# Performance work log

Hardware: AMD Instinct MI355X
Metric: run time of the kernel (lower is better)

The kernel has to match this reference:

```python
import jax, jax.numpy as jnp
import numpy as np

B, S, D, H, L = 32, 1024, 512, 8, 4
DH = D // H
FF = D            # dim_feedforward == hidden_dim in the original ctor call
LOC_D, TD_D = 16, 8
TD_EMB = 3        # time_dist_embed_dim
POI = 21          # poi vocab
POI_EMB = 3
ADDR_IN = 1 + POI_EMB
FC = 32           # fc_hidden_dim
NEG = -1e9


def setup_inputs() -> dict:
    key = jax.random.key(0)
    ks = jax.random.split(key, 20)
    g = lambda i, shape, s=0.02: jax.random.normal(ks[i], shape, jnp.float32) * s
    return {
        "addr": jax.random.normal(ks[0], (B, 1), jnp.float32),
        "loc_dense_seq": jax.random.normal(ks[1], (B, S, LOC_D), jnp.float32),
        "time_dist_seq": jax.random.normal(ks[2], (B, S, TD_D), jnp.float32),
        "Wtd": g(3, (TD_D, TD_EMB)), "btd": jnp.zeros((TD_EMB,), jnp.float32),
        "Wemb": g(4, (LOC_D + TD_EMB, D)), "bemb": jnp.zeros((D,), jnp.float32),
        "Wqkv": g(5, (L, D, 3 * D)), "bqkv": jnp.zeros((L, 3 * D), jnp.float32),
        "Wo": g(6, (L, D, D)), "bo": jnp.zeros((L, D), jnp.float32),
        "ln1_g": jnp.ones((L, D), jnp.float32), "ln1_b": jnp.zeros((L, D), jnp.float32),
        "W1": g(7, (L, D, FF)), "b1": jnp.zeros((L, FF), jnp.float32),
        "W2": g(8, (L, FF, D)), "b2": jnp.zeros((L, D), jnp.float32),
        "ln2_g": jnp.ones((L, D), jnp.float32), "ln2_b": jnp.zeros((L, D), jnp.float32),
        "poi_emb": g(9, (POI, POI_EMB), 1.0),
        "Wa": g(10, (ADDR_IN, FC)), "ba": jnp.zeros((FC,), jnp.float32),
        "Wout": g(11, (D, FC)),
        "Wcomb": g(12, (FC, 1)),
        "addr_type": jax.random.randint(ks[13], (B, 1), 0, POI),
        "data_length": jax.random.randint(ks[14], (B,), 1, S + 1),
    }


def _ln(x, g, b, eps=1e-5):
    m = x.mean(-1, keepdims=True)
    v = ((x - m) ** 2).mean(-1, keepdims=True)
    return (x - m) / jnp.sqrt(v + eps) * g + b


def reference(addr, loc_dense_seq, time_dist_seq, Wtd, btd, Wemb, bemb, Wqkv,
              bqkv, Wo, bo, ln1_g, ln1_b, W1, b1, W2, b2, ln2_g, ln2_b,
              poi_emb, Wa, ba, Wout, Wcomb, addr_type, data_length):
    valid = jnp.arange(S)[None, :] < data_length[:, None]            # [B,S]
    td = time_dist_seq @ Wtd + btd                                   # [B,S,3]
    x = jnp.concatenate([loc_dense_seq, td], axis=-1) @ Wemb + bemb  # [B,S,D]
    scale = 1.0 / jnp.sqrt(jnp.float32(DH))
    for l in range(L):  # post-norm TransformerEncoderLayer (relu, eval/no-dropout)
        qkv = x @ Wqkv[l] + bqkv[l]
        q, k, v = jnp.split(qkv, 3, axis=-1)
        q = q.reshape(B, S, H, DH)
        k = k.reshape(B, S, H, DH)
        v = v.reshape(B, S, H, DH)
        scores = jnp.einsum('bqhd,bkhd->bhqk', q, k) * scale
        scores = jnp.where(valid[:, None, None, :], scores, NEG)     # mask padded keys
        attn = jax.nn.softmax(scores, axis=-1)
        ctx = jnp.einsum('bhqk,bkhd->bqhd', attn, v).reshape(B, S, D)
        x = _ln(x + ctx @ Wo[l] + bo[l], ln1_g[l], ln1_b[l])
        ff = jax.nn.relu(x @ W1[l] + b1[l]) @ W2[l] + b2[l]
        x = _ln(x + ff, ln2_g[l], ln2_b[l])
    # per-sample addr branch (vectorized over the original python loop)
    addr_inp = jnp.concatenate([addr, poi_emb[addr_type[:, 0]]], axis=-1)  # [B,4]
    a = addr_inp @ Wa + ba                                                 # [B,FC]
    o = (jnp.tanh(x @ Wout + a[:, None, :]) @ Wcomb)[..., 0]              # [B,S]
    logits = jnp.where(valid, o, NEG)
    logp = jax.nn.log_softmax(logits, axis=1)  # log_softmax over valid positions only
    return jnp.where(valid, logp, 0.0)
```

## Files before the change

### kernel.cpp

```cpp
#include <hip/hip_runtime.h>
#include <stdint.h>


typedef unsigned short u16;
typedef __attribute__((ext_vector_type(8))) short short8;
typedef __attribute__((ext_vector_type(4))) float f32x4;

constexpr int Bn = 32, Sn = 1024, Dn = 512, Ln = 4;
constexpr int BS = Bn * Sn;

__device__ __forceinline__ float b2f(u16 u) {
    union { uint32_t i; float f; } v; v.i = ((uint32_t)u) << 16; return v.f;
}
__device__ __forceinline__ u16 f2b(float f) {
    union { float f; uint32_t i; } v; v.f = f;
    uint32_t r = v.i + 0x7fffu + ((v.i >> 16) & 1u);
    return (u16)(r >> 16);
}
__device__ __forceinline__ float getf(const void* p, size_t i, int F) {
    return F ? ((const float*)p)[i] : b2f(((const u16*)p)[i]);
}
__device__ __forceinline__ void cp16(void* lds, const void* g) {
    __builtin_amdgcn_global_load_lds(
        (__attribute__((address_space(1))) void*)(uintptr_t)g,
        (__attribute__((address_space(3))) void*)(uint32_t)(uintptr_t)lds,
        16, 0, 0);
}
__device__ __forceinline__ float asf(uint32_t u) {
    union { uint32_t i; float f; } v; v.i = u; return v.f;
}

__global__ __launch_bounds__(256)
void detect_kernel(const void* loc, int* flag)
{
    __shared__ int cnt;
    if (threadIdx.x == 0) cnt = 0;
    __syncthreads();
    const u16* p = (const u16*)loc;
    int c = 0;
    for (int i = threadIdx.x; i < 2048; i += 256) {
        const float v = b2f(p[i]);
        if (!(fabsf(v) <= 100.0f)) c++;
    }
    atomicAdd(&cnt, c);
    __syncthreads();
    if (threadIdx.x == 0) *flag = (cnt >= 64) ? 1 : 0;
}

__global__ __launch_bounds__(256)
void gemm_bt(const u16* __restrict__ A, const u16* __restrict__ Bt,
             const void* __restrict__ bias, int boff, u16* __restrict__ C,
             int N, int K, int relu, const int* __restrict__ flagp,
             const int* __restrict__ dlen)
{
    __shared__ __align__(16) u16 As[128 * 32];
    __shared__ __align__(16) u16 Bs[128 * 32];
    const int bn0 = blockIdx.x * 128, bm0 = blockIdx.y * 128;
    if ((bm0 & 1023) >= dlen[bm0 >> 10]) return;
    const int F = *flagp;
    const int tid = threadIdx.x;
    const int lane = tid & 63, w = tid >> 6;
    const int wm = w >> 1, wn = w & 1;
    const int quad = lane >> 4, l16 = lane & 15;

    const f32x4 vzero = {0.f, 0.f, 0.f, 0.f};
    f32x4 acc[4][4];
#pragma unroll
    for (int i = 0; i < 4; i++)
#pragma unroll
        for (int j = 0; j < 4; j++) acc[i][j] = vzero;

    const int i0 = tid, i1 = tid + 256;
    const u16* a0 = A + (size_t)(bm0 + (i0 >> 2)) * K + (i0 & 3) * 8;
    const u16* a1 = A + (size_t)(bm0 + (i1 >> 2)) * K + (i1 & 3) * 8;
    const u16* b0 = Bt + (size_t)(bn0 + (i0 >> 2)) * K + (i0 & 3) * 8;
    const u16* b1 = Bt + (size_t)(bn0 + (i1 >> 2)) * K + (i1 & 3) * 8;

    for (int k0 = 0; k0 < K; k0 += 32) {
        cp16(As + i0 * 8, a0 + k0);
        cp16(As + i1 * 8, a1 + k0);
        cp16(Bs + i0 * 8, b0 + k0);
        cp16(Bs + i1 * 8, b1 + k0);
        __syncthreads();
        short8 af[4], bfr[4];
#pragma unroll
        for (int t = 0; t < 4; t++)
            af[t] = *(const short8*)&As[(wm * 64 + t * 16 + l16) * 32 + quad * 8];
#pragma unroll
        for (int t = 0; t < 4; t++)
            bfr[t] = *(const short8*)&Bs[(wn * 64 + t * 16 + l16) * 32 + quad * 8];
#pragma unroll
        for (int tm = 0; tm < 4; tm++)
#pragma unroll
            for (int tn = 0; tn < 4; tn++)
                acc[tm][tn] = __builtin_amdgcn_mfma_f32_16x16x32_bf16(
                    af[tm], bfr[tn], acc[tm][tn], 0, 0, 0);
        __syncthreads();
    }
#pragma unroll
    for (int tm = 0; tm < 4; tm++)
#pragma unroll
        for (int tn = 0; tn < 4; tn++) {
            const int col = bn0 + wn * 64 + tn * 16 + l16;
            const float bv = getf(bias, (size_t)boff + col, F);
#pragma unroll
            for (int r = 0; r < 4; r++) {
                const int row = bm0 + wm * 64 + tm * 16 + quad * 4 + r;
                float v = acc[tm][tn][r] + bv;
                if (relu) v = fmaxf(v, 0.0f);
                C[(size_t)row * N + col] = f2b(v);
            }
        }
}

__global__ __launch_bounds__(256)
void attn_kernel(const u16* __restrict__ qkv, const int* __restrict__ dlen,
                 u16* __restrict__ ctx)
{
    const int id = blockIdx.x;
    const int qt = id >> 8, bh = id & 255;
    const int h = bh & 7, b = bh >> 3;
    const int len = dlen[b];
    if (qt * 128 >= len) return;
    const int tid = threadIdx.x, lane = tid & 63, w = tid >> 6;
    const int quad = lane >> 4, l16 = lane & 15;
    __shared__ __align__(16) u16 Vt[2][64 * 72];
    __shared__ __align__(16) u16 Pl[4][32 * 72];
    u16* Plw = Pl[w];
    const int sw = l16 & 3;
    const size_t rs = 3 * Dn;
    const u16* base = qkv + (size_t)b * Sn * rs;
    const int q0 = qt * 128 + w * 32;
    constexpr float SC = 0.18033688011112043f;

    short8 qf[2][2];
#pragma unroll
    for (int sub = 0; sub < 2; sub++)
#pragma unroll
        for (int s = 0; s < 2; s++)
            qf[sub][s] = *(const short8*)(base + (size_t)(q0 + sub * 16 + l16) * rs
                                          + h * 64 + quad * 8 + 32 * s);

    const int key2 = (tid & 31) * 2, f0 = (tid >> 5) * 8;
    const u16* vsrc = base + 2 * Dn + h * 64 + f0;
    short8 v0 = *(const short8*)(vsrc + (size_t)key2 * rs);
    short8 v1 = *(const short8*)(vsrc + (size_t)(key2 + 1) * rs);

    short8 ones;
#pragma unroll
    for (int j = 0; j < 8; j++) ones[j] = (short)0x3F80;

    const f32x4 vzero = {0.f, 0.f, 0.f, 0.f};
    f32x4 O[2][4], lacc[2];
#pragma unroll
    for (int sub = 0; sub < 2; sub++) {
        lacc[sub] = vzero;
#pragma unroll
        for (int t = 0; t < 4; t++) O[sub][t] = vzero;
    }

    const int nkt = (len + 63) >> 6;
    int buf = 0;
    for (int kt = 0; kt < nkt; kt++) {
        const int k0 = kt * 64;
        u16* Vb = Vt[buf];
#pragma unroll
        for (int j = 0; j < 8; j++)
            *(uint32_t*)&Vb[(f0 + j) * 72 + key2] =
                (uint32_t)(u16)v0[j] | ((uint32_t)(u16)v1[j] << 16);
        __syncthreads();
        if (kt + 1 < nkt) {
            const u16* nv = vsrc + (size_t)(k0 + 64 + key2) * rs;
            v0 = *(const short8*)nv;
            v1 = *(const short8*)(nv + rs);
        }
        short8 kf[4][2];
#pragma unroll
        for (int tn = 0; tn < 4; tn++) {
            const u16* kp = base + (size_t)(k0 + tn * 16 + l16) * rs + Dn
                            + h * 64 + quad * 8;
            kf[tn][0] = *(const short8*)kp;
            kf[tn][1] = *(const short8*)(kp + 32);
        }
        const bool full = (k0 + 64 <= len);
#pragma unroll
        for (int sub = 0; sub < 2; sub++) {
            f32x4 sacc[4];
#pragma unroll
            for (int tn = 0; tn < 4; tn++) {
                f32x4 z = vzero;
                z = __builtin_amdgcn_mfma_f32_16x16x32_bf16(kf[tn][0], qf[sub][0], z, 0, 0, 0);
                sacc[tn] = __builtin_amdgcn_mfma_f32_16x16x32_bf16(kf[tn][1], qf[sub][1], z, 0, 0, 0);
            }
            const int prow = (sub * 16 + l16) * 72;
#pragma unroll
            for (int tn = 0; tn < 4; tn++) {
                float p[4];
                if (full) {
#pragma unroll
                    for (int r = 0; r < 4; r++) p[r] = exp2f(sacc[tn][r] * SC);
                } else {
                    const int kb = k0 + tn * 16 + quad * 4;
#pragma unroll
                    for (int r = 0; r < 4; r++)
                        p[r] = (kb + r < len) ? exp2f(sacc[tn][r] * SC) : 0.0f;
                }
                uint2 pk;
                pk.x = (__float_as_uint(p[0]) >> 16) | (__float_as_uint(p[1]) & 0xFFFF0000u);
                pk.y = (__float_as_uint(p[2]) >> 16) | (__float_as_uint(p[3]) & 0xFFFF0000u);
                *(uint2*)&Plw[prow + (((tn ^ sw) << 4) + quad * 4)] = pk;
            }
        }
        __builtin_amdgcn_wave_barrier();
#pragma unroll
        for (int s = 0; s < 2; s++) {
            const int tnr = ((quad >> 1) + 2 * s) ^ sw;
            short8 pf0 = *(const short8*)&Plw[(l16) * 72 + (tnr << 4) + (quad & 1) * 8];
            short8 pf1 = *(const short8*)&Plw[(16 + l16) * 72 + (tnr << 4) + (quad & 1) * 8];
            lacc[0] = __builtin_amdgcn_mfma_f32_16x16x32_bf16(pf0, ones, lacc[0], 0, 0, 0);
            lacc[1] = __builtin_amdgcn_mfma_f32_16x16x32_bf16(pf1, ones, lacc[1], 0, 0, 0);
#pragma unroll
            for (int t = 0; t < 4; t++) {
                short8 vf = *(const short8*)&Vb[(t * 16 + l16) * 72 + quad * 8 + 32 * s];
                O[0][t] = __builtin_amdgcn_mfma_f32_16x16x32_bf16(pf0, vf, O[0][t], 0, 0, 0);
                O[1][t] = __builtin_amdgcn_mfma_f32_16x16x32_bf16(pf1, vf, O[1][t], 0, 0, 0);
            }
        }
        __builtin_amdgcn_wave_barrier();
        buf ^= 1;
    }
#pragma unroll
    for (int sub = 0; sub < 2; sub++)
#pragma unroll
        for (int r = 0; r < 4; r++) {
            const float inv = 1.0f / lacc[sub][r];
            const int q = q0 + sub * 16 + quad * 4 + r;
#pragma unroll
            for (int t = 0; t < 4; t++)
                ctx[(size_t)(b * Sn + q) * Dn + h * 64 + t * 16 + l16] =
                    f2b(O[sub][t][r] * inv);
        }
}

__global__ __launch_bounds__(256)
void ln_res(u16* __restrict__ x, const u16* __restrict__ t,
            const void* __restrict__ g, const void* __restrict__ bta, int off,
            const int* __restrict__ flagp, const int* __restrict__ dlen)
{
    const int w = threadIdx.x >> 6, lane = threadIdx.x & 63;
    const size_t row = (size_t)blockIdx.x * 4 + w;
    if ((int)(row & 1023) >= dlen[row >> 10]) return;
    const int F = *flagp;
    u16* xp = x + row * Dn;
    const u16* tp = t + row * Dn;
    const int c0 = lane * 8;
    short8 xv = *(const short8*)(xp + c0);
    short8 tv = *(const short8*)(tp + c0);
    float v[8]; float s = 0.f;
#pragma unroll
    for (int i = 0; i < 8; i++) {
        v[i] = b2f((u16)xv[i]) + b2f((u16)tv[i]);
        s += v[i];
    }
#pragma unroll
    for (int o = 1; o < 64; o <<= 1) s += __shfl_xor(s, o, 64);
    const float mean = s * (1.0f / 512.0f);
    float q = 0.f;
#pragma unroll
    for (int i = 0; i < 8; i++) { const float d = v[i] - mean; q += d * d; }
#pragma unroll
    for (int o = 1; o < 64; o <<= 1) q += __shfl_xor(q, o, 64);
    const float inv = rsqrtf(q * (1.0f / 512.0f) + 1e-5f);
    short8 ov;
#pragma unroll
    for (int i = 0; i < 8; i++)
        ov[i] = (short)f2b((v[i] - mean) * inv * getf(g, off + c0 + i, F)
                           + getf(bta, off + c0 + i, F));
    *(short8*)(xp + c0) = ov;
}

__global__ __launch_bounds__(256)
void embed_kernel(const void* __restrict__ loc, const void* __restrict__ tds,
                  const void* __restrict__ Wtd, const void* __restrict__ btd,
                  const void* __restrict__ Wemb, const void* __restrict__ bemb,
                  u16* __restrict__ x, const int* __restrict__ flagp,
                  const int* __restrict__ dlen)
{
    const int token = blockIdx.x;
    if ((token & 1023) >= dlen[token >> 10]) return;
    const int F = *flagp;
    const int tid = threadIdx.x;
    __shared__ float inv[19];
    if (tid < 16) {
        inv[tid] = getf(loc, (size_t)token * 16 + tid, F);
    } else if (tid < 19) {
        const int e = tid - 16;
        float a = getf(btd, e, F);
        for (int j = 0; j < 8; j++)
            a += getf(tds, (size_t)token * 8 + j, F) * getf(Wtd, j * 3 + e, F);
        inv[tid] = a;
    }
    __syncthreads();
    for (int d = tid; d < Dn; d += 256) {
        float a = getf(bemb, d, F);
#pragma unroll
        for (int i = 0; i < 19; i++) a += inv[i] * getf(Wemb, (size_t)i * Dn + d, F);
        x[(size_t)token * Dn + d] = f2b(a);
    }
}

__global__ __launch_bounds__(256)
void transpose_w(const void* __restrict__ src, u16* __restrict__ dst,
                 int K, int N, const int* __restrict__ flagp)
{
    const int F = *flagp;
    __shared__ u16 tile[32][33];
    const size_t ls = (size_t)K * N;
    const size_t sb = (size_t)blockIdx.z * ls;
    u16* d = dst + blockIdx.z * ls;
    const int tx = threadIdx.x & 31, ty = threadIdx.x >> 5;
    const int n0 = blockIdx.x * 32, k0 = blockIdx.y * 32;
#pragma unroll
    for (int i = 0; i < 32; i += 8)
        tile[ty + i][tx] = f2b(getf(src, sb + (size_t)(k0 + ty + i) * N + n0 + tx, F));
    __syncthreads();
#pragma unroll
    for (int i = 0; i < 32; i += 8)
        d[(size_t)(n0 + ty + i) * K + k0 + tx] = tile[tx][ty + i];
}

__global__ __launch_bounds__(256)
void final_proj(const u16* __restrict__ x, const void* __restrict__ Wout,
                const void* __restrict__ Wcomb, const void* __restrict__ addr,
                const void* __restrict__ poi, const int* __restrict__ atype,
                const void* __restrict__ Wa, const void* __restrict__ ba,
                float* __restrict__ logits, const int* __restrict__ flagp,
                const int* __restrict__ dlen)
{
    const int F = *flagp;
    __shared__ float xs[8][512];
    __shared__ __align__(8) u16 wlds[32 * 516];
    const int tid = threadIdx.x;
    const int t0 = blockIdx.x * 8;
    for (int i = tid; i < 8 * 512; i += 256) {
        const int tk = i >> 9, d = i & 511;
        xs[tk][d] = b2f(x[(size_t)(t0 + tk) * Dn + d]);
    }
    for (int i = tid; i < 16384; i += 256) {
        const int k = i >> 5, j = i & 31;
        wlds[j * 516 + k] = F ? f2b(((const float*)Wout)[(size_t)k * 32 + j])
                              : ((const u16*)Wout)[(size_t)k * 32 + j];
    }
    __syncthreads();
    const int half = tid >> 5, j = tid & 31;
    const int token = t0 + half;
    const int b = token >> 10;
    if ((token & 1023) >= dlen[b]) return;
    const int ty = atype[b];
    float a = getf(ba, j, F) + getf(addr, b, F) * getf(Wa, j, F);
#pragma unroll
    for (int e = 0; e < 3; e++)
        a += getf(poi, ty * 3 + e, F) * getf(Wa, (1 + e) * 32 + j, F);
    float s = a;
    const u16* wj = wlds + j * 516;
    const float* xr = xs[half];
#pragma unroll 4
    for (int k = 0; k < 512; k += 4) {
        const uint2 wv = *(const uint2*)&wj[k];
        s += xr[k]     * asf(wv.x << 16);
        s += xr[k + 1] * asf(wv.x & 0xFFFF0000u);
        s += xr[k + 2] * asf(wv.y << 16);
        s += xr[k + 3] * asf(wv.y & 0xFFFF0000u);
    }
    float o = tanhf(s) * getf(Wcomb, j, F);
#pragma unroll
    for (int off = 1; off < 32; off <<= 1) o += __shfl_xor(o, off, 64);
    if (j == 0) logits[token] = o;
}

__global__ __launch_bounds__(256)
void lsm_kernel(const float* __restrict__ logits, const int* __restrict__ dlen,
                float* __restrict__ out)
{
    const int b = blockIdx.x, tid = threadIdx.x;
    const int len = dlen[b];
    const float* lp = logits + (size_t)b * Sn;
    __shared__ float wA[4], wB[4];
    float mx = -3e38f;
    for (int s = tid; s < Sn; s += 256) if (s < len) mx = fmaxf(mx, lp[s]);
#pragma unroll
    for (int o = 1; o < 64; o <<= 1) mx = fmaxf(mx, __shfl_xor(mx, o, 64));
    if ((tid & 63) == 0) wA[tid >> 6] = mx;
    __syncthreads();
    mx = fmaxf(fmaxf(wA[0], wA[1]), fmaxf(wA[2], wA[3]));
    float sm = 0.f;
    for (int s = tid; s < Sn; s += 256) if (s < len) sm += __expf(lp[s] - mx);
#pragma unroll
    for (int o = 1; o < 64; o <<= 1) sm += __shfl_xor(sm, o, 64);
    if ((tid & 63) == 0) wB[tid >> 6] = sm;
    __syncthreads();
    const float lse = mx + __logf(wB[0] + wB[1] + wB[2] + wB[3]);
    for (int s = tid; s < Sn; s += 256)
        out[(size_t)b * Sn + s] = (s < len) ? (lp[s] - lse) : 0.0f;
}

extern "C" void kernel_launch(void* const* d_in, const int* in_sizes, int n_in,
                              void* d_out, int out_size, void* d_ws, size_t ws_size,
                              hipStream_t stream) {
    const void* addr  = d_in[0];
    const void* loc   = d_in[1];
    const void* tds   = d_in[2];
    const void* Wtd   = d_in[3];
    const void* btd   = d_in[4];
    const void* Wemb  = d_in[5];
    const void* bemb  = d_in[6];
    const void* Wqkv  = d_in[7];
    const void* bqkv  = d_in[8];
    const void* Wo    = d_in[9];
    const void* bo    = d_in[10];
    const void* ln1g  = d_in[11];
    const void* ln1b  = d_in[12];
    const void* W1    = d_in[13];
    const void* b1    = d_in[14];
    const void* W2    = d_in[15];
    const void* b2    = d_in[16];
    const void* ln2g  = d_in[17];
    const void* ln2b  = d_in[18];
    const void* poi   = d_in[19];
    const void* Wa    = d_in[20];
    const void* ba    = d_in[21];
    const void* Wout  = d_in[22];
    const void* Wcomb = d_in[23];
    const int* atype  = (const int*)d_in[24];
    const int* dlen   = (const int*)d_in[25];

    char* base = (char*)d_ws;
    u16*   xb    = (u16*)(base);
    u16*   qkvb  = (u16*)(base + 33554432ull);
    u16*   ctxb  = (u16*)(base + 134217728ull);
    u16*   tb    = (u16*)(base + 167772160ull);
    u16*   wqkvT = (u16*)(base + 201326592ull);
    u16*   woT   = (u16*)(base + 207618048ull);
    u16*   w1T   = (u16*)(base + 209715200ull);
    u16*   w2T   = (u16*)(base + 211812352ull);
    float* logit = (float*)(base + 213909504ull);
    int*   flag  = (int*)  (base + 214040576ull);
    if (ws_size < 214040592ull) return;

    detect_kernel<<<1, 256, 0, stream>>>(loc, flag);

    transpose_w<<<dim3(48, 16, 4), 256, 0, stream>>>(Wqkv, wqkvT, 512, 1536, flag);
    transpose_w<<<dim3(16, 16, 4), 256, 0, stream>>>(Wo,   woT,   512, 512, flag);
    transpose_w<<<dim3(16, 16, 4), 256, 0, stream>>>(W1,   w1T,   512, 512, flag);
    transpose_w<<<dim3(16, 16, 4), 256, 0, stream>>>(W2,   w2T,   512, 512, flag);

    embed_kernel<<<BS, 256, 0, stream>>>(loc, tds, Wtd, btd, Wemb, bemb, xb, flag, dlen);

    for (int l = 0; l < Ln; l++) {
        gemm_bt<<<dim3(12, 256), 256, 0, stream>>>(
            xb, wqkvT + (size_t)l * 1536 * 512, bqkv, l * 1536, qkvb, 1536, 512, 0, flag, dlen);
        attn_kernel<<<2048, 256, 0, stream>>>(qkvb, dlen, ctxb);
        gemm_bt<<<dim3(4, 256), 256, 0, stream>>>(
            ctxb, woT + (size_t)l * 512 * 512, bo, l * 512, tb, 512, 512, 0, flag, dlen);
        ln_res<<<BS / 4, 256, 0, stream>>>(xb, tb, ln1g, ln1b, l * 512, flag, dlen);
        gemm_bt<<<dim3(4, 256), 256, 0, stream>>>(
            xb, w1T + (size_t)l * 512 * 512, b1, l * 512, ctxb, 512, 512, 1, flag, dlen);
        gemm_bt<<<dim3(4, 256), 256, 0, stream>>>(
            ctxb, w2T + (size_t)l * 512 * 512, b2, l * 512, tb, 512, 512, 0, flag, dlen);
        ln_res<<<BS / 4, 256, 0, stream>>>(xb, tb, ln2g, ln2b, l * 512, flag, dlen);
    }

    final_proj<<<BS / 8, 256, 0, stream>>>(xb, Wout, Wcomb, addr, poi, atype,
                                           Wa, ba, logit, flag, dlen);
    lsm_kernel<<<Bn, 256, 0, stream>>>(logit, dlen, (float*)d_out);
}
```

Before: 1.747 ms.

## Prefetch K fragments one tile ahead, reverse query-tile order, skip padded final blocks

The attention kernel now double-buffers K fragments in registers, loading the next key tile's K alongside the V prefetch so global-load latency overlaps the current tile's MFMA work. Query tiles are dispatched in reverse order so the longest-running tiles start first, which improves load balance across the variable sequence lengths. The final projection kernel returns early for blocks whose first token lies past the valid length, so no shared-memory staging is done for them. The K double buffer raises register pressure and may reduce occupancy.

```diff
diff --git a/kernel.cpp b/kernel.cpp
--- a/kernel.cpp
+++ b/kernel.cpp
@@ -118,7 +118,8 @@
                  u16* __restrict__ ctx)
 {
     const int id = blockIdx.x;
-    const int qt = id >> 8, bh = id & 255;
+    const int qt = 7 - (id >> 8);
+    const int bh = id & 255;
     const int h = bh & 7, b = bh >> 3;
     const int len = dlen[b];
     if (qt * 128 >= len) return;
@@ -146,6 +147,15 @@
     short8 v0 = *(const short8*)(vsrc + (size_t)key2 * rs);
     short8 v1 = *(const short8*)(vsrc + (size_t)(key2 + 1) * rs);
 
+    const u16* kbase = base + Dn + h * 64 + quad * 8;
+    short8 kfb[2][4][2];
+#pragma unroll
+    for (int tn = 0; tn < 4; tn++) {
+        const u16* kp = kbase + (size_t)(tn * 16 + l16) * rs;
+        kfb[0][tn][0] = *(const short8*)kp;
+        kfb[0][tn][1] = *(const short8*)(kp + 32);
+    }
+
     short8 ones;
 #pragma unroll
     for (int j = 0; j < 8; j++) ones[j] = (short)0x3F80;
@@ -160,7 +170,7 @@
     }
 
     const int nkt = (len + 63) >> 6;
-    int buf = 0;
+    int buf = 0, kb = 0;
     for (int kt = 0; kt < nkt; kt++) {
         const int k0 = kt * 64;
         u16* Vb = Vt[buf];
@@ -173,14 +183,12 @@
             const u16* nv = vsrc + (size_t)(k0 + 64 + key2) * rs;
             v0 = *(const short8*)nv;
             v1 = *(const short8*)(nv + rs);
-        }
-        short8 kf[4][2];
-#pragma unroll
-        for (int tn = 0; tn < 4; tn++) {
-            const u16* kp = base + (size_t)(k0 + tn * 16 + l16) * rs + Dn
-                            + h * 64 + quad * 8;
-            kf[tn][0] = *(const short8*)kp;
-            kf[tn][1] = *(const short8*)(kp + 32);
+#pragma unroll
+            for (int tn = 0; tn < 4; tn++) {
+                const u16* kp = kbase + (size_t)(k0 + 64 + tn * 16 + l16) * rs;
+                kfb[kb ^ 1][tn][0] = *(const short8*)kp;
+                kfb[kb ^ 1][tn][1] = *(const short8*)(kp + 32);
+            }
         }
         const bool full = (k0 + 64 <= len);
 #pragma unroll
@@ -189,8 +197,8 @@
 #pragma unroll
             for (int tn = 0; tn < 4; tn++) {
                 f32x4 z = vzero;
-                z = __builtin_amdgcn_mfma_f32_16x16x32_bf16(kf[tn][0], qf[sub][0], z, 0, 0, 0);
-                sacc[tn] = __builtin_amdgcn_mfma_f32_16x16x32_bf16(kf[tn][1], qf[sub][1], z, 0, 0, 0);
+                z = __builtin_amdgcn_mfma_f32_16x16x32_bf16(kfb[kb][tn][0], qf[sub][0], z, 0, 0, 0);
+                sacc[tn] = __builtin_amdgcn_mfma_f32_16x16x32_bf16(kfb[kb][tn][1], qf[sub][1], z, 0, 0, 0);
             }
             const int prow = (sub * 16 + l16) * 72;
 #pragma unroll
@@ -200,10 +208,10 @@
 #pragma unroll
                     for (int r = 0; r < 4; r++) p[r] = exp2f(sacc[tn][r] * SC);
                 } else {
-                    const int kb = k0 + tn * 16 + quad * 4;
+                    const int kbnd = k0 + tn * 16 + quad * 4;
 #pragma unroll
                     for (int r = 0; r < 4; r++)
-                        p[r] = (kb + r < len) ? exp2f(sacc[tn][r] * SC) : 0.0f;
+                        p[r] = (kbnd + r < len) ? exp2f(sacc[tn][r] * SC) : 0.0f;
                 }
                 uint2 pk;
                 pk.x = (__float_as_uint(p[0]) >> 16) | (__float_as_uint(p[1]) & 0xFFFF0000u);
@@ -228,6 +236,7 @@
         }
         __builtin_amdgcn_wave_barrier();
         buf ^= 1;
+        kb ^= 1;
     }
 #pragma unroll
     for (int sub = 0; sub < 2; sub++)
@@ -337,11 +346,12 @@
                 float* __restrict__ logits, const int* __restrict__ flagp,
                 const int* __restrict__ dlen)
 {
+    const int t0 = blockIdx.x * 8;
+    if ((t0 & 1023) >= dlen[t0 >> 10]) return;
     const int F = *flagp;
     __shared__ float xs[8][512];
     __shared__ __align__(8) u16 wlds[32 * 516];
     const int tid = threadIdx.x;
-    const int t0 = blockIdx.x * 8;
     for (int i = tid; i < 8 * 512; i += 256) {
         const int tk = i >> 9, d = i & 511;
         xs[tk][d] = b2f(x[(size_t)(t0 + tk) * Dn + d]);
```

Result: slower. 2.297 ms (+31.4%).

## Write QKV in head-major layout and reverse attention query-tile order

Applied to the files above, without the earlier changes.

The QKV GEMM epilogue now scatters Q, K and V into separate per-(batch, head) contiguous [S,64] buffers instead of interleaved 1536-wide rows, so attention loads read 128-byte contiguous rows rather than strided slices. Attention blocks are launched with the heaviest query tiles first to improve load balance, and final_proj skips blocks whose tokens are all padding. The scattered epilogue stores become narrower per row (2-byte strided writes), which may cost write coalescing in the GEMM.

```diff
diff --git a/kernel.cpp b/kernel.cpp
--- a/kernel.cpp
+++ b/kernel.cpp
@@ -8,6 +8,7 @@
 
 constexpr int Bn = 32, Sn = 1024, Dn = 512, Ln = 4;
 constexpr int BS = Bn * Sn;
+constexpr size_t QKV_OFF = 16777216;
 
 __device__ __forceinline__ float b2f(u16 u) {
     union { uint32_t i; float f; } v; v.i = ((uint32_t)u) << 16; return v.f;
@@ -50,7 +51,7 @@
 __global__ __launch_bounds__(256)
 void gemm_bt(const u16* __restrict__ A, const u16* __restrict__ Bt,
              const void* __restrict__ bias, int boff, u16* __restrict__ C,
-             int N, int K, int relu, const int* __restrict__ flagp,
+             int N, int K, int relu, int mode, const int* __restrict__ flagp,
              const int* __restrict__ dlen)
 {
     __shared__ __align__(16) u16 As[128 * 32];
@@ -97,28 +98,43 @@
                     af[tm], bfr[tn], acc[tm][tn], 0, 0, 0);
         __syncthreads();
     }
+    const int bb = bm0 >> 10;
 #pragma unroll
     for (int tm = 0; tm < 4; tm++)
 #pragma unroll
         for (int tn = 0; tn < 4; tn++) {
             const int col = bn0 + wn * 64 + tn * 16 + l16;
             const float bv = getf(bias, (size_t)boff + col, F);
-#pragma unroll
-            for (int r = 0; r < 4; r++) {
-                const int row = bm0 + wm * 64 + tm * 16 + quad * 4 + r;
-                float v = acc[tm][tn][r] + bv;
-                if (relu) v = fmaxf(v, 0.0f);
-                C[(size_t)row * N + col] = f2b(v);
+            if (mode == 0) {
+#pragma unroll
+                for (int r = 0; r < 4; r++) {
+                    const int row = bm0 + wm * 64 + tm * 16 + quad * 4 + r;
+                    float v = acc[tm][tn][r] + bv;
+                    if (relu) v = fmaxf(v, 0.0f);
+                    C[(size_t)row * N + col] = f2b(v);
+                }
+            } else {
+                const int which = col >> 9;
+                const int c = col & 511;
+                const int hh = c >> 6, f = c & 63;
+                u16* dst = C + (size_t)which * QKV_OFF
+                           + (((size_t)(bb * 8 + hh)) << 16) + f;
+#pragma unroll
+                for (int r = 0; r < 4; r++) {
+                    const int s = (bm0 & 1023) + wm * 64 + tm * 16 + quad * 4 + r;
+                    dst[(size_t)s * 64] = f2b(acc[tm][tn][r] + bv);
+                }
             }
         }
 }
 
 __global__ __launch_bounds__(256)
-void attn_kernel(const u16* __restrict__ qkv, const int* __restrict__ dlen,
+void attn_kernel(const u16* __restrict__ qp, const int* __restrict__ dlen,
                  u16* __restrict__ ctx)
 {
     const int id = blockIdx.x;
-    const int qt = id >> 8, bh = id & 255;
+    const int qt = 7 - (id >> 8);
+    const int bh = id & 255;
     const int h = bh & 7, b = bh >> 3;
     const int len = dlen[b];
     if (qt * 128 >= len) return;
@@ -128,8 +144,9 @@
     __shared__ __align__(16) u16 Pl[4][32 * 72];
     u16* Plw = Pl[w];
     const int sw = l16 & 3;
-    const size_t rs = 3 * Dn;
-    const u16* base = qkv + (size_t)b * Sn * rs;
+    const u16* qb = qp + ((size_t)bh << 16);
+    const u16* kb = qb + QKV_OFF;
+    const u16* vb = qb + 2 * QKV_OFF;
     const int q0 = qt * 128 + w * 32;
     constexpr float SC = 0.18033688011112043f;
 
@@ -138,13 +155,13 @@
     for (int sub = 0; sub < 2; sub++)
 #pragma unroll
         for (int s = 0; s < 2; s++)
-            qf[sub][s] = *(const short8*)(base + (size_t)(q0 + sub * 16 + l16) * rs
-                                          + h * 64 + quad * 8 + 32 * s);
+            qf[sub][s] = *(const short8*)(qb + (size_t)(q0 + sub * 16 + l16) * 64
+                                          + quad * 8 + 32 * s);
 
     const int key2 = (tid & 31) * 2, f0 = (tid >> 5) * 8;
-    const u16* vsrc = base + 2 * Dn + h * 64 + f0;
-    short8 v0 = *(const short8*)(vsrc + (size_t)key2 * rs);
-    short8 v1 = *(const short8*)(vsrc + (size_t)(key2 + 1) * rs);
+    const u16* vsrc = vb + f0;
+    short8 v0 = *(const short8*)(vsrc + (size_t)key2 * 64);
+    short8 v1 = *(const short8*)(vsrc + (size_t)(key2 + 1) * 64);
 
     short8 ones;
 #pragma unroll
@@ -170,17 +187,16 @@
                 (uint32_t)(u16)v0[j] | ((uint32_t)(u16)v1[j] << 16);
         __syncthreads();
         if (kt + 1 < nkt) {
-            const u16* nv = vsrc + (size_t)(k0 + 64 + key2) * rs;
+            const u16* nv = vsrc + (size_t)(k0 + 64 + key2) * 64;
             v0 = *(const short8*)nv;
-            v1 = *(const short8*)(nv + rs);
+            v1 = *(const short8*)(nv + 64);
         }
         short8 kf[4][2];
 #pragma unroll
         for (int tn = 0; tn < 4; tn++) {
-            const u16* kp = base + (size_t)(k0 + tn * 16 + l16) * rs + Dn
-                            + h * 64 + quad * 8;
-            kf[tn][0] = *(const short8*)kp;
-            kf[tn][1] = *(const short8*)(kp + 32);
+            const u16* kp2 = kb + (size_t)(k0 + tn * 16 + l16) * 64 + quad * 8;
+            kf[tn][0] = *(const short8*)kp2;
+            kf[tn][1] = *(const short8*)(kp2 + 32);
         }
         const bool full = (k0 + 64 <= len);
 #pragma unroll
@@ -200,10 +216,10 @@
 #pragma unroll
                     for (int r = 0; r < 4; r++) p[r] = exp2f(sacc[tn][r] * SC);
                 } else {
-                    const int kb = k0 + tn * 16 + quad * 4;
+                    const int kbnd = k0 + tn * 16 + quad * 4;
 #pragma unroll
                     for (int r = 0; r < 4; r++)
-                        p[r] = (kb + r < len) ? exp2f(sacc[tn][r] * SC) : 0.0f;
+                        p[r] = (kbnd + r < len) ? exp2f(sacc[tn][r] * SC) : 0.0f;
                 }
                 uint2 pk;
                 pk.x = (__float_as_uint(p[0]) >> 16) | (__float_as_uint(p[1]) & 0xFFFF0000u);
@@ -337,11 +353,12 @@
                 float* __restrict__ logits, const int* __restrict__ flagp,
                 const int* __restrict__ dlen)
 {
+    const int t0 = blockIdx.x * 8;
+    if ((t0 & 1023) >= dlen[t0 >> 10]) return;
     const int F = *flagp;
     __shared__ float xs[8][512];
     __shared__ __align__(8) u16 wlds[32 * 516];
     const int tid = threadIdx.x;
-    const int t0 = blockIdx.x * 8;
     for (int i = tid; i < 8 * 512; i += 256) {
         const int tk = i >> 9, d = i & 511;
         xs[tk][d] = b2f(x[(size_t)(t0 + tk) * Dn + d]);
@@ -436,7 +453,7 @@
 
     char* base = (char*)d_ws;
     u16*   xb    = (u16*)(base);
-    u16*   qkvb  = (u16*)(base + 33554432ull);
+    u16*   qkvp  = (u16*)(base + 33554432ull);
     u16*   ctxb  = (u16*)(base + 134217728ull);
     u16*   tb    = (u16*)(base + 167772160ull);
     u16*   wqkvT = (u16*)(base + 201326592ull);
@@ -458,15 +475,15 @@
 
     for (int l = 0; l < Ln; l++) {
         gemm_bt<<<dim3(12, 256), 256, 0, stream>>>(
-            xb, wqkvT + (size_t)l * 1536 * 512, bqkv, l * 1536, qkvb, 1536, 512, 0, flag, dlen);
-        attn_kernel<<<2048, 256, 0, stream>>>(qkvb, dlen, ctxb);
+            xb, wqkvT + (size_t)l * 1536 * 512, bqkv, l * 1536, qkvp, 1536, 512, 0, 1, flag, dlen);
+        attn_kernel<<<2048, 256, 0, stream>>>(qkvp, dlen, ctxb);
         gemm_bt<<<dim3(4, 256), 256, 0, stream>>>(
-            ctxb, woT + (size_t)l * 512 * 512, bo, l * 512, tb, 512, 512, 0, flag, dlen);
+            ctxb, woT + (size_t)l * 512 * 512, bo, l * 512, tb, 512, 512, 0, 0, flag, dlen);
         ln_res<<<BS / 4, 256, 0, stream>>>(xb, tb, ln1g, ln1b, l * 512, flag, dlen);
         gemm_bt<<<dim3(4, 256), 256, 0, stream>>>(
-            xb, w1T + (size_t)l * 512 * 512, b1, l * 512, ctxb, 512, 512, 1, flag, dlen);
+            xb, w1T + (size_t)l * 512 * 512, b1, l * 512, ctxb, 512, 512, 1, 0, flag, dlen);
         gemm_bt<<<dim3(4, 256), 256, 0, stream>>>(
-            ctxb, w2T + (size_t)l * 512 * 512, b2, l * 512, tb, 512, 512, 0, flag, dlen);
+            ctxb, w2T + (size_t)l * 512 * 512, b2, l * 512, tb, 512, 512, 0, 0, flag, dlen);
         ln_res<<<BS / 4, 256, 0, stream>>>(xb, tb, ln2g, ln2b, l * 512, flag, dlen);
     }
 
```

After: 1.737 ms. About the same (-0.6%).
